# Optimization experiments

Hardware: AMD Instinct MI355X
Metric: run time of the kernel (lower is better)

## Reference

```python
import jax, jax.numpy as jnp
import numpy as np

NUM_BINS = 15
NUM_CLASSES = 4
NEIGHBORHOOD_WIDTH = 3  # K; num_neighbor_classes = K**2 = 9


def _neighbor_counts(onehot):
    """Count of same-class neighbors in KxK window (center excluded), zero padding.
    onehot: [B, C, H, W] float32 one-hot of hard predictions.
    returns int32 [B, C, H, W] in [0, K^2-1].
    """
    K = NEIGHBORHOOD_WIDTH
    C = onehot.shape[1]
    kern = np.ones((K, K), dtype=np.float32)
    kern[K // 2, K // 2] = 0.0  # exclude center pixel
    kernel = jnp.asarray(np.broadcast_to(kern, (C, 1, K, K)).copy())  # depthwise OIHW
    counts = jax.lax.conv_general_dilated(
        onehot, kernel,
        window_strides=(1, 1), padding='SAME',
        feature_group_count=C,
        dimension_numbers=('NCHW', 'OIHW', 'NCHW'))
    return jnp.clip(jnp.round(counts).astype(jnp.int32), 0, K * K - 1)


def setup_inputs() -> dict:
    key = jax.random.key(0)
    k1, k2 = jax.random.split(key)
    logits = jax.random.normal(k1, (16, NUM_CLASSES, 512, 512), dtype=jnp.float32)
    # calibration frequency table: val_freqs[class][neighbor_count][conf_bin]
    val_freqs = jax.random.uniform(k2, (NUM_CLASSES, NEIGHBORHOOD_WIDTH ** 2, NUM_BINS), dtype=jnp.float32)
    return {"logits": logits, "val_freqs": val_freqs}


def reference(logits, val_freqs):
    B, C, H, W = logits.shape
    probs = jax.nn.softmax(logits, axis=1)                      # [B,C,H,W]
    y_hard = jnp.argmax(probs, axis=1)                          # [B,H,W]

    # (y_hard == lab_idx) for every class at once -> one-hot [B,C,H,W]
    onehot = jax.nn.one_hot(y_hard, C, axis=1, dtype=jnp.float32)
    agg = _neighbor_counts(onehot)                              # [B,C,H,W] int32 in [0, K^2-1]

    # confidence bin per pixel/class: uniform bins on [0,1]
    bin_width = 1.0 / NUM_BINS
    bin_map = jnp.clip((probs / bin_width).astype(jnp.int32), 0, NUM_BINS - 1)  # [B,C,H,W]

    # fused multi-index gather replacing the nested class/neighbor-mask loops:
    # calibrated[b,c,h,w] = val_freqs[c, agg[b,c,h,w], bin_map[b,c,h,w]]
    cls_idx = jnp.arange(C, dtype=jnp.int32)[None, :, None, None]
    calibrated = val_freqs[cls_idx, agg, bin_map]               # [B,C,H,W]

    # normalize across classes, guarding zero sums
    s = jnp.sum(calibrated, axis=1, keepdims=True)
    s = jnp.where(s == 0, 1.0, s)
    return calibrated / s
```

## Files before the change

### kernel.cpp

```cpp
#include <hip/hip_runtime.h>

#define HW (512 * 512)

typedef float vfloat4 __attribute__((ext_vector_type(4)));

constexpr float BWIDTH = 1.0f / 15.0f;
constexpr float DELTA = 3e-5f;

__global__ __launch_bounds__(256) void nectar_binning_kernel(
    const float* __restrict__ logits,
    const float* __restrict__ val_freqs,
    float* __restrict__ out)
{
    __shared__ float vf[540];

    const int tid  = (int)threadIdx.x;
    const int lane = tid & 63;
    const int wv   = tid >> 6;

    float vfr[9];
    #pragma unroll
    for (int i = 0; i < 9; i++) {
        int idx = 64 * i + lane;
        vfr[i] = (idx < 540) ? val_freqs[idx] : 0.f;
    }

    const unsigned bi  = blockIdx.x;
    const unsigned bsw = ((bi & 7u) << 7) | (bi >> 3);
    const int seg = (int)(4u * bsw) + wv;
    const int b   = seg >> 8;
    const int grp = seg & 255;
    const int h0  = grp << 1;

    const float* lb = logits + (size_t)b * 4 * HW;
    float*       ob = out    + (size_t)b * 4 * HW;
    const int colA = 4 * lane;
    const int colB = 256 + 4 * lane;

    auto LOADROW = [&](vfloat4 (&dst)[4][2], int r) {
        const float* rp = lb + (r << 9);
        #pragma unroll
        for (int c = 0; c < 4; c++) {
            dst[c][0] = *reinterpret_cast<const vfloat4*>(rp + (size_t)c * HW + colA);
            dst[c][1] = *reinterpret_cast<const vfloat4*>(rp + (size_t)c * HW + colB);
        }
    };

    auto NIBROW = [&](const vfloat4 (&x)[4][2], unsigned (&N)[2][2]) {
        #pragma unroll
        for (int h = 0; h < 2; h++) {
            unsigned n[4];
            #pragma unroll
            for (int j = 0; j < 4; j++) {
                float x0 = x[0][h][j], x1 = x[1][h][j], x2 = x[2][h][j], x3 = x[3][h][j];
                int c = 0; float best = x0;
                if (x1 > best) { best = x1; c = 1; }
                if (x2 > best) { best = x2; c = 2; }
                if (x3 > best) { best = x3; c = 3; }
                n[j] = 1u << (4 * c);
            }
            N[h][0] = n[0] | (n[1] << 16);
            N[h][1] = n[2] | (n[3] << 16);
        }
    };

    auto NIBPBROW = [&](const vfloat4 (&x)[4][2], unsigned (&N)[2][2], unsigned (&P)[2][2]) {
        #pragma unroll
        for (int h = 0; h < 2; h++) {
            unsigned n[4], pbv[4];
            #pragma unroll
            for (int j = 0; j < 4; j++) {
                float x0 = x[0][h][j], x1 = x[1][h][j], x2 = x[2][h][j], x3 = x[3][h][j];
                int c = 0; float best = x0;
                if (x1 > best) { best = x1; c = 1; }
                if (x2 > best) { best = x2; c = 2; }
                if (x3 > best) { best = x3; c = 3; }
                n[j] = 1u << (4 * c);

                float m = fmaxf(fmaxf(x0, x1), fmaxf(x2, x3));
                float t0 = x0 - m, t1 = x1 - m, t2 = x2 - m, t3 = x3 - m;
                float f0 = __expf(t0), f1 = __expf(t1), f2 = __expf(t2), f3 = __expf(t3);
                float sf = ((f0 + f1) + f2) + f3;
                float rs = __builtin_amdgcn_rcpf(sf);
                float q[4];
                q[0] = (f0 * rs) * 15.0f; q[1] = (f1 * rs) * 15.0f;
                q[2] = (f2 * rs) * 15.0f; q[3] = (f3 * rs) * 15.0f;
                bool slow = false;
                #pragma unroll
                for (int c2 = 0; c2 < 4; c2++) {
                    float fr = q[c2] - floorf(q[c2]);
                    slow |= (fr < DELTA) | (fr > 1.0f - DELTA);
                }
                if (slow) {
                    float e0 = expf(t0), e1 = expf(t1), e2 = expf(t2), e3 = expf(t3);
                    float s = ((e0 + e1) + e2) + e3;
                    q[0] = (e0 / s) / BWIDTH; q[1] = (e1 / s) / BWIDTH;
                    q[2] = (e2 / s) / BWIDTH; q[3] = (e3 / s) / BWIDTH;
                }
                unsigned pb = 0;
                #pragma unroll
                for (int c2 = 0; c2 < 4; c2++) {
                    int bin = (int)q[c2];
                    bin = bin > 14 ? 14 : bin;
                    pb |= (unsigned)bin << (4 * c2);
                }
                pbv[j] = pb;
            }
            N[h][0] = n[0]   | (n[1]   << 16);
            N[h][1] = n[2]   | (n[3]   << 16);
            P[h][0] = pbv[0] | (pbv[1] << 16);
            P[h][1] = pbv[2] | (pbv[3] << 16);
        }
    };

    auto OUTROW = [&](int r, const unsigned (&T)[2][2], const unsigned (&M)[2][2],
                      const unsigned (&B)[2][2], const unsigned (&P)[2][2]) {
        unsigned C[2][2];
        #pragma unroll
        for (int h = 0; h < 2; h++) {
            C[h][0] = T[h][0] + M[h][0] + B[h][0];
            C[h][1] = T[h][1] + M[h][1] + B[h][1];
        }
        unsigned upA = __shfl_up(C[0][1], 1) >> 16;   if (lane == 0)  upA = 0;
        unsigned ebA = __shfl(C[0][1], 63) >> 16;
        unsigned upB = __shfl_up(C[1][1], 1) >> 16;   if (lane == 0)  upB = ebA;
        unsigned e0B = __shfl(C[1][0], 0) & 0xFFFFu;
        unsigned dnA = __shfl_down(C[0][0], 1) & 0xFFFFu; if (lane == 63) dnA = e0B;
        unsigned dnB = __shfl_down(C[1][0], 1) & 0xFFFFu; if (lane == 63) dnB = 0;
        const unsigned up[2] = {upA, upB}, dn[2] = {dnA, dnB};

        float res[4][2][4];
        #pragma unroll
        for (int h = 0; h < 2; h++) {
            unsigned L0 = (C[h][0] << 16) | up[h];
            unsigned R0 = (C[h][0] >> 16) | (C[h][1] << 16);
            unsigned R1 = (C[h][1] >> 16) | (dn[h] << 16);
            unsigned PKw[2];
            PKw[0] = C[h][0] + L0 + R0 - M[h][0];
            PKw[1] = C[h][1] + R0 + R1 - M[h][1];
            #pragma unroll
            for (int j = 0; j < 4; j++) {
                unsigned pk = (PKw[j >> 1]  >> (16 * (j & 1))) & 0xFFFFu;
                unsigned pb = (P[h][j >> 1] >> (16 * (j & 1))) & 0xFFFFu;
                float cs = 0.0f;
                float cal[4];
                #pragma unroll
                for (int c = 0; c < 4; c++) {
                    int cnt = (int)((pk >> (4 * c)) & 0xFu);
                    int bin = (int)((pb >> (4 * c)) & 0xFu);
                    float v = vf[c * 135 + cnt * 15 + bin];
                    cal[c] = v;
                    cs += v;
                }
                if (cs == 0.0f) cs = 1.0f;
                float inv = __builtin_amdgcn_rcpf(cs);
                #pragma unroll
                for (int c = 0; c < 4; c++) res[c][h][j] = cal[c] * inv;
            }
        }
        float* rp = ob + (r << 9);
        #pragma unroll
        for (int c = 0; c < 4; c++) {
            vfloat4 v0; v0.x = res[c][0][0]; v0.y = res[c][0][1]; v0.z = res[c][0][2]; v0.w = res[c][0][3];
            vfloat4 v1; v1.x = res[c][1][0]; v1.y = res[c][1][1]; v1.z = res[c][1][2]; v1.w = res[c][1][3];
            __builtin_nontemporal_store(v0, reinterpret_cast<vfloat4*>(rp + (size_t)c * HW + colA));
            __builtin_nontemporal_store(v1, reinterpret_cast<vfloat4*>(rp + (size_t)c * HW + colB));
        }
    };

    auto ROT = [&](unsigned (&T)[2][2], unsigned (&M)[2][2], const unsigned (&B)[2][2],
                   unsigned (&PC)[2][2], const unsigned (&PN)[2][2]) {
        #pragma unroll
        for (int h = 0; h < 2; h++)
            #pragma unroll
            for (int k = 0; k < 2; k++) {
                T[h][k] = M[h][k]; M[h][k] = B[h][k]; PC[h][k] = PN[h][k];
            }
    };

    vfloat4 U[4][2], V[4][2];
    unsigned T[2][2], M[2][2], B[2][2], PC[2][2], PN[2][2];

    LOADROW(U, (grp > 0) ? (h0 - 1) : 0);
    LOADROW(V, h0);
    #pragma unroll
    for (int i = 0; i < 9; i++) {
        int idx = 64 * i + lane;
        if (idx < 540) vf[idx] = vfr[i];
    }
    NIBROW(U, T);
    if (grp == 0) { T[0][0] = T[0][1] = T[1][0] = T[1][1] = 0; }
    LOADROW(U, h0 + 1);
    NIBPBROW(V, M, PC);
    LOADROW(V, (grp < 255) ? (h0 + 2) : 511);

    NIBPBROW(U, B, PN);
    OUTROW(h0, T, M, B, PC);
    ROT(T, M, B, PC, PN);

    NIBROW(V, B);
    if (grp == 255) { B[0][0] = B[0][1] = B[1][0] = B[1][1] = 0; }
    OUTROW(h0 + 1, T, M, B, PC);
}

extern "C" void kernel_launch(void* const* d_in, const int* in_sizes, int n_in,
                              void* d_out, int out_size, void* d_ws, size_t ws_size,
                              hipStream_t stream) {
    const float* logits    = (const float*)d_in[0];
    const float* val_freqs = (const float*)d_in[1];
    float* out             = (float*)d_out;

    dim3 block(256, 1, 1);
    dim3 grid(1024, 1, 1);
    hipLaunchKernelGGL(nectar_binning_kernel, grid, block, 0, stream,
                       logits, val_freqs, out);
}
```

Measured before the change: 118.7 us.

## Process one row per wave and recompute table lookups to cut registers

Each wave now handles a single output row instead of two, which doubles the grid and raises halo reloads from 2x to 3x per output row. A single shared input buffer replaces the two row buffers, and the calibrated values are re-read from shared memory at store time instead of kept in registers. A launch-bounds occupancy hint is added. The aim is more waves in flight to hide memory latency, paid for with extra global loads for neighbor rows and duplicated LDS lookups.

```diff
diff --git a/kernel.cpp b/kernel.cpp
--- a/kernel.cpp
+++ b/kernel.cpp
@@ -7,7 +7,7 @@
 constexpr float BWIDTH = 1.0f / 15.0f;
 constexpr float DELTA = 3e-5f;
 
-__global__ __launch_bounds__(256) void nectar_binning_kernel(
+__global__ __launch_bounds__(256, 7) void nectar_binning_kernel(
     const float* __restrict__ logits,
     const float* __restrict__ val_freqs,
     float* __restrict__ out)
@@ -26,27 +26,27 @@
     }
 
     const unsigned bi  = blockIdx.x;
-    const unsigned bsw = ((bi & 7u) << 7) | (bi >> 3);
+    const unsigned bsw = ((bi & 7u) << 8) | (bi >> 3);
     const int seg = (int)(4u * bsw) + wv;
-    const int b   = seg >> 8;
-    const int grp = seg & 255;
-    const int h0  = grp << 1;
+    const int b   = seg >> 9;
+    const int row = seg & 511;
 
     const float* lb = logits + (size_t)b * 4 * HW;
     float*       ob = out    + (size_t)b * 4 * HW;
     const int colA = 4 * lane;
     const int colB = 256 + 4 * lane;
 
-    auto LOADROW = [&](vfloat4 (&dst)[4][2], int r) {
+    vfloat4 x[4][2];
+    auto LOADROW = [&](int r) {
         const float* rp = lb + (r << 9);
         #pragma unroll
         for (int c = 0; c < 4; c++) {
-            dst[c][0] = *reinterpret_cast<const vfloat4*>(rp + (size_t)c * HW + colA);
-            dst[c][1] = *reinterpret_cast<const vfloat4*>(rp + (size_t)c * HW + colB);
+            x[c][0] = *reinterpret_cast<const vfloat4*>(rp + (size_t)c * HW + colA);
+            x[c][1] = *reinterpret_cast<const vfloat4*>(rp + (size_t)c * HW + colB);
         }
     };
 
-    auto NIBROW = [&](const vfloat4 (&x)[4][2], unsigned (&N)[2][2]) {
+    auto NIBROW = [&](unsigned (&N)[2][2]) {
         #pragma unroll
         for (int h = 0; h < 2; h++) {
             unsigned n[4];
@@ -64,7 +64,7 @@
         }
     };
 
-    auto NIBPBROW = [&](const vfloat4 (&x)[4][2], unsigned (&N)[2][2], unsigned (&P)[2][2]) {
+    auto NIBPBROW = [&](unsigned (&N)[2][2], unsigned (&P)[2][2]) {
         #pragma unroll
         for (int h = 0; h < 2; h++) {
             unsigned n[4], pbv[4];
@@ -113,94 +113,85 @@
         }
     };
 
-    auto OUTROW = [&](int r, const unsigned (&T)[2][2], const unsigned (&M)[2][2],
-                      const unsigned (&B)[2][2], const unsigned (&P)[2][2]) {
-        unsigned C[2][2];
-        #pragma unroll
-        for (int h = 0; h < 2; h++) {
-            C[h][0] = T[h][0] + M[h][0] + B[h][0];
-            C[h][1] = T[h][1] + M[h][1] + B[h][1];
-        }
-        unsigned upA = __shfl_up(C[0][1], 1) >> 16;   if (lane == 0)  upA = 0;
-        unsigned ebA = __shfl(C[0][1], 63) >> 16;
-        unsigned upB = __shfl_up(C[1][1], 1) >> 16;   if (lane == 0)  upB = ebA;
-        unsigned e0B = __shfl(C[1][0], 0) & 0xFFFFu;
-        unsigned dnA = __shfl_down(C[0][0], 1) & 0xFFFFu; if (lane == 63) dnA = e0B;
-        unsigned dnB = __shfl_down(C[1][0], 1) & 0xFFFFu; if (lane == 63) dnB = 0;
-        const unsigned up[2] = {upA, upB}, dn[2] = {dnA, dnB};
-
-        float res[4][2][4];
-        #pragma unroll
-        for (int h = 0; h < 2; h++) {
-            unsigned L0 = (C[h][0] << 16) | up[h];
-            unsigned R0 = (C[h][0] >> 16) | (C[h][1] << 16);
-            unsigned R1 = (C[h][1] >> 16) | (dn[h] << 16);
-            unsigned PKw[2];
-            PKw[0] = C[h][0] + L0 + R0 - M[h][0];
-            PKw[1] = C[h][1] + R0 + R1 - M[h][1];
-            #pragma unroll
-            for (int j = 0; j < 4; j++) {
-                unsigned pk = (PKw[j >> 1]  >> (16 * (j & 1))) & 0xFFFFu;
-                unsigned pb = (P[h][j >> 1] >> (16 * (j & 1))) & 0xFFFFu;
-                float cs = 0.0f;
-                float cal[4];
-                #pragma unroll
-                for (int c = 0; c < 4; c++) {
-                    int cnt = (int)((pk >> (4 * c)) & 0xFu);
-                    int bin = (int)((pb >> (4 * c)) & 0xFu);
-                    float v = vf[c * 135 + cnt * 15 + bin];
-                    cal[c] = v;
-                    cs += v;
-                }
-                if (cs == 0.0f) cs = 1.0f;
-                float inv = __builtin_amdgcn_rcpf(cs);
-                #pragma unroll
-                for (int c = 0; c < 4; c++) res[c][h][j] = cal[c] * inv;
-            }
-        }
-        float* rp = ob + (r << 9);
-        #pragma unroll
-        for (int c = 0; c < 4; c++) {
-            vfloat4 v0; v0.x = res[c][0][0]; v0.y = res[c][0][1]; v0.z = res[c][0][2]; v0.w = res[c][0][3];
-            vfloat4 v1; v1.x = res[c][1][0]; v1.y = res[c][1][1]; v1.z = res[c][1][2]; v1.w = res[c][1][3];
-            __builtin_nontemporal_store(v0, reinterpret_cast<vfloat4*>(rp + (size_t)c * HW + colA));
-            __builtin_nontemporal_store(v1, reinterpret_cast<vfloat4*>(rp + (size_t)c * HW + colB));
-        }
-    };
-
-    auto ROT = [&](unsigned (&T)[2][2], unsigned (&M)[2][2], const unsigned (&B)[2][2],
-                   unsigned (&PC)[2][2], const unsigned (&PN)[2][2]) {
-        #pragma unroll
-        for (int h = 0; h < 2; h++)
-            #pragma unroll
-            for (int k = 0; k < 2; k++) {
-                T[h][k] = M[h][k]; M[h][k] = B[h][k]; PC[h][k] = PN[h][k];
-            }
-    };
-
-    vfloat4 U[4][2], V[4][2];
-    unsigned T[2][2], M[2][2], B[2][2], PC[2][2], PN[2][2];
-
-    LOADROW(U, (grp > 0) ? (h0 - 1) : 0);
-    LOADROW(V, h0);
+    unsigned T[2][2], M[2][2], B[2][2], PC[2][2];
+
+    LOADROW(row > 0 ? row - 1 : 0);
     #pragma unroll
     for (int i = 0; i < 9; i++) {
         int idx = 64 * i + lane;
         if (idx < 540) vf[idx] = vfr[i];
     }
-    NIBROW(U, T);
-    if (grp == 0) { T[0][0] = T[0][1] = T[1][0] = T[1][1] = 0; }
-    LOADROW(U, h0 + 1);
-    NIBPBROW(V, M, PC);
-    LOADROW(V, (grp < 255) ? (h0 + 2) : 511);
-
-    NIBPBROW(U, B, PN);
-    OUTROW(h0, T, M, B, PC);
-    ROT(T, M, B, PC, PN);
-
-    NIBROW(V, B);
-    if (grp == 255) { B[0][0] = B[0][1] = B[1][0] = B[1][1] = 0; }
-    OUTROW(h0 + 1, T, M, B, PC);
+    NIBROW(T);
+    if (row == 0) { T[0][0] = T[0][1] = T[1][0] = T[1][1] = 0; }
+
+    LOADROW(row);
+    NIBPBROW(M, PC);
+
+    LOADROW(row < 511 ? row + 1 : 511);
+    NIBROW(B);
+    if (row == 511) { B[0][0] = B[0][1] = B[1][0] = B[1][1] = 0; }
+
+    unsigned C[2][2];
+    #pragma unroll
+    for (int h = 0; h < 2; h++) {
+        C[h][0] = T[h][0] + M[h][0] + B[h][0];
+        C[h][1] = T[h][1] + M[h][1] + B[h][1];
+    }
+    unsigned upA = __shfl_up(C[0][1], 1) >> 16;   if (lane == 0)  upA = 0;
+    unsigned ebA = __shfl(C[0][1], 63) >> 16;
+    unsigned upB = __shfl_up(C[1][1], 1) >> 16;   if (lane == 0)  upB = ebA;
+    unsigned e0B = __shfl(C[1][0], 0) & 0xFFFFu;
+    unsigned dnA = __shfl_down(C[0][0], 1) & 0xFFFFu; if (lane == 63) dnA = e0B;
+    unsigned dnB = __shfl_down(C[1][0], 1) & 0xFFFFu; if (lane == 63) dnB = 0;
+    const unsigned up[2] = {upA, upB}, dn[2] = {dnA, dnB};
+
+    unsigned PKw[2][2];
+    #pragma unroll
+    for (int h = 0; h < 2; h++) {
+        unsigned L0 = (C[h][0] << 16) | up[h];
+        unsigned R0 = (C[h][0] >> 16) | (C[h][1] << 16);
+        unsigned R1 = (C[h][1] >> 16) | (dn[h] << 16);
+        PKw[h][0] = C[h][0] + L0 + R0 - M[h][0];
+        PKw[h][1] = C[h][1] + R0 + R1 - M[h][1];
+    }
+
+    float inv[2][4];
+    #pragma unroll
+    for (int h = 0; h < 2; h++) {
+        #pragma unroll
+        for (int j = 0; j < 4; j++) {
+            unsigned pk = (PKw[h][j >> 1] >> (16 * (j & 1))) & 0xFFFFu;
+            unsigned pb = (PC[h][j >> 1] >> (16 * (j & 1))) & 0xFFFFu;
+            float cs = 0.0f;
+            #pragma unroll
+            for (int c = 0; c < 4; c++) {
+                int cnt = (int)((pk >> (4 * c)) & 0xFu);
+                int bin = (int)((pb >> (4 * c)) & 0xFu);
+                cs += vf[c * 135 + cnt * 15 + bin];
+            }
+            if (cs == 0.0f) cs = 1.0f;
+            inv[h][j] = __builtin_amdgcn_rcpf(cs);
+        }
+    }
+
+    float* rp = ob + (row << 9);
+    #pragma unroll
+    for (int c = 0; c < 4; c++) {
+        vfloat4 v0, v1;
+        #pragma unroll
+        for (int j = 0; j < 4; j++) {
+            unsigned pk0 = (PKw[0][j >> 1] >> (16 * (j & 1))) & 0xFFFFu;
+            unsigned pb0 = (PC[0][j >> 1] >> (16 * (j & 1))) & 0xFFFFu;
+            v0[j] = vf[c * 135 + (int)((pk0 >> (4 * c)) & 0xFu) * 15
+                               + (int)((pb0 >> (4 * c)) & 0xFu)] * inv[0][j];
+            unsigned pk1 = (PKw[1][j >> 1] >> (16 * (j & 1))) & 0xFFFFu;
+            unsigned pb1 = (PC[1][j >> 1] >> (16 * (j & 1))) & 0xFFFFu;
+            v1[j] = vf[c * 135 + (int)((pk1 >> (4 * c)) & 0xFu) * 15
+                               + (int)((pb1 >> (4 * c)) & 0xFu)] * inv[1][j];
+        }
+        __builtin_nontemporal_store(v0, reinterpret_cast<vfloat4*>(rp + (size_t)c * HW + colA));
+        __builtin_nontemporal_store(v1, reinterpret_cast<vfloat4*>(rp + (size_t)c * HW + colB));
+    }
 }
 
 extern "C" void kernel_launch(void* const* d_in, const int* in_sizes, int n_in,
@@ -211,7 +202,7 @@
     float* out             = (float*)d_out;
 
     dim3 block(256, 1, 1);
-    dim3 grid(1024, 1, 1);
+    dim3 grid(2048, 1, 1);
     hipLaunchKernelGGL(nectar_binning_kernel, grid, block, 0, stream,
                        logits, val_freqs, out);
 }
```

Measured after the change: 187.1 us. 1.58x slower.
